# Optimization experiments

Hardware: AMD Instinct MI355X
Metric: run time of the kernel (lower is better)

Reference implementation:

```python
import jax, jax.numpy as jnp
import numpy as np

B, L, D = 4, 2048, 768
K, M, CK = 12, 1, 4            # heads, thetas, conv kernel size
H = D // (K * M)               # 64
DIM_MEM = K * H                # 768
DIM_EXPAND = H * 3             # 192
DSH = DIM_EXPAND * 2           # 384 swiglu head dim
DST = K * DSH                  # 4608
DIM_FUSED = DIM_MEM + K + DST  # 5388
THETA_MIN, THETA_MAX = 1e-3, 3.0


def setup_inputs() -> dict:
    key = jax.random.key(0)
    ks = jax.random.split(key, 5)
    x = jax.random.normal(ks[0], (B, L, D), jnp.float32)
    W_in = jax.random.normal(ks[1], (D, DIM_FUSED), jnp.float32) * 0.02
    conv_w = jax.random.normal(ks[2], (CK, DIM_MEM + K), jnp.float32) * 0.2  # depthwise taps
    rms_scale = jnp.ones((H,), jnp.float32)
    # theta_raw init (M==1 branch): inverse-sigmoid of geomspace grid
    grid = np.geomspace(THETA_MIN, THETA_MAX, K).reshape(1, 1, K, 1, 1)
    base = np.tile(grid, (1, 1, 1, H, 1))
    u = np.clip((base - THETA_MIN) / (THETA_MAX - THETA_MIN), 1e-4, 1 - 1e-4)
    theta_raw = jnp.asarray(np.log(u) - np.log(1.0 - u), jnp.float32)
    decay_slopes = jnp.asarray(np.log(np.exp(np.geomspace(1e-3, 0.1, K)) - 1.0), jnp.float32)
    score_scale = jnp.ones((K,), jnp.float32)
    tanh_scale = jnp.ones((K,), jnp.float32)
    W_sw = jax.random.normal(ks[3], (2 * K * H * M, DST), jnp.float32) * 0.02
    W_out = jax.random.normal(ks[4], (K * DIM_EXPAND, D), jnp.float32) * 0.02
    return {"x": x, "W_in": W_in, "conv_w": conv_w, "rms_scale": rms_scale,
            "theta_raw": theta_raw, "decay_slopes": decay_slopes,
            "score_scale": score_scale, "tanh_scale": tanh_scale,
            "W_sw": W_sw, "W_out": W_out}


def reference(x, W_in, conv_w, rms_scale, theta_raw, decay_slopes,
              score_scale, tanh_scale, W_sw, W_out):
    # fused in-projection
    z_fused = jnp.einsum('bld,df->blf', x, W_in)
    z_mem = z_fused[..., :DIM_MEM + K]
    skip_direct = z_fused[..., DIM_MEM + K:]
    # causal depthwise conv (kernel size CK, left pad CK-1)
    zp = jnp.pad(z_mem, ((0, 0), (CK - 1, 0), (0, 0)))
    z_conv = sum(zp[:, j:j + L, :] * conv_w[j] for j in range(CK))
    z_mem = jax.nn.silu(z_conv)
    # memory keys + RMSNorm over H
    k_val = z_mem[..., :DIM_MEM].reshape(B, L, K, H)
    k_val = k_val * jax.lax.rsqrt(jnp.mean(k_val * k_val, axis=-1, keepdims=True) + 1e-6) * rms_scale
    s_raw = z_mem[..., DIM_MEM:]  # (B, L, K)
    # theta (M == 1)
    theta = THETA_MIN + (THETA_MAX - THETA_MIN) * jax.nn.sigmoid(theta_raw)  # (1,1,K,H,1)
    # decay time weights (num_anchor_heads == 0, maxlen == L)
    pos = jnp.arange(L, dtype=jnp.float32)
    slopes = jax.nn.softplus(decay_slopes).reshape(1, 1, K)
    dist = jnp.maximum(jnp.float32(L - 1) - pos, 0.0)
    log_time_weight = -slopes * dist[None, :, None]  # (1, L, K)
    log_p = jnp.clip(score_scale[None, None, :] * s_raw, -10.0, 10.0)
    p_w = jnp.exp(log_p + log_time_weight)  # (B, L, K)
    # characteristic-function encoding
    k5 = k_val[..., None]  # (B, L, K, H, 1)
    phi = jnp.tanh(k5 * tanh_scale.reshape(1, 1, K, 1, 1)) * theta
    kvw = k5 * p_w[..., None, None]
    re = kvw * jnp.cos(phi)
    im = kvw * jnp.sin(phi)
    # fused causal cumulative accumulation
    flat = K * H * M
    stack = jnp.concatenate([p_w, re.reshape(B, L, flat), im.reshape(B, L, flat)], axis=-1)
    cs = jnp.cumsum(stack, axis=1)
    den_acc = cs[..., :K]
    re_acc = cs[..., K:K + flat].reshape(B, L, K, H, M)
    im_acc = cs[..., K + flat:].reshape(B, L, K, H, M)
    inv_den = (1.0 / jnp.maximum(den_acc, 1e-4))[..., None, None]
    summary_flat = jnp.stack([re_acc * inv_den, im_acc * inv_den], axis=-1).reshape(B, L, -1)
    # SwiGLU with skip
    y_spectral = jnp.einsum('bls,sf->blf', summary_flat, W_sw).reshape(B, L, K, DSH)
    y_skip = skip_direct.reshape(B, L, K, DSH)
    y_spec_val, y_spec_gate = jnp.split(y_spectral, 2, axis=-1)
    y_skip_val, y_skip_gate = jnp.split(y_skip, 2, axis=-1)
    y_act = (y_spec_val + y_skip_val) * jax.nn.silu(y_spec_gate + y_skip_gate)
    out = jnp.einsum('blf,fd->bld', y_act.reshape(B, L, -1), W_out)
    return out
```

## Files before the change

kernel.cpp:

```cpp
#include <hip/hip_runtime.h>
#include <hip/hip_bf16.h>

#define B_       4
#define L_       2048
#define D_       768
#define K_       12
#define H_       64
#define CK_      4
#define DIM_MEM_ 768
#define DMK      780
#define NT       (B_*L_)
#define NSUM     1536
#define NACT     2304
#define NCHUNK   16
#define CHLEN    (L_/NCHUNK)
#define PSTRIDE  132

typedef __attribute__((ext_vector_type(8))) short          bf16x8;
typedef __attribute__((ext_vector_type(8))) unsigned short u16x8;
typedef __attribute__((ext_vector_type(4))) float          f32x4;

__device__ __forceinline__ ushort f2bf(float v) {
    __hip_bfloat16 h = __float2bfloat16(v);
    return *reinterpret_cast<ushort*>(&h);
}
__device__ __forceinline__ float tanh_fast(float x) {
    float t = __expf(-2.f * fabsf(x));
    float r = (1.f - t) / (1.f + t);
    return copysignf(r, x);
}

struct PrepJobs {
    const float* W[6];
    ushort*      out[6];
    int ldw[6], Kd[6], colbase[6], remap[6], ntx[6];
    int start[7];
    const float* cast_in;
    ushort*      cast_out;
    int n4;
};

__global__ __launch_bounds__(256)
void prep_all(PrepJobs J)
{
    int blk = blockIdx.x;
    if (blk >= J.start[6]) {
        int i = (blk - J.start[6]) * 256 + threadIdx.x;
        if (i < J.n4) {
            float4 v = reinterpret_cast<const float4*>(J.cast_in)[i];
            ushort4 o;
            o.x = f2bf(v.x); o.y = f2bf(v.y); o.z = f2bf(v.z); o.w = f2bf(v.w);
            reinterpret_cast<ushort4*>(J.cast_out)[i] = o;
        }
        return;
    }
    int j = 0;
    while (blk >= J.start[j + 1]) ++j;
    int rel = blk - J.start[j];
    int ntx = J.ntx[j];
    int n0 = (rel % ntx) * 32, k0 = (rel / ntx) * 32;
    const float* W = J.W[j];
    int ldw = J.ldw[j], Kd = J.Kd[j], colbase = J.colbase[j], remap = J.remap[j];
    ushort* out = J.out[j];

    __shared__ float tile[32][33];
    int tx = threadIdx.x & 31, ty = threadIdx.x >> 5;
    int n = n0 + tx;
    int c = colbase + (remap ? (n/192)*384 + (n%192) : n);
    #pragma unroll
    for (int r = 0; r < 4; ++r)
        tile[ty + r*8][tx] = W[(size_t)(k0 + ty + r*8) * ldw + c];
    __syncthreads();
    #pragma unroll
    for (int r = 0; r < 4; ++r)
        out[(size_t)(n0 + ty + r*8) * Kd + k0 + tx] = f2bf(tile[tx][ty + r*8]);
}

__global__ __launch_bounds__(256)
void gemm_bf16_mfma(const ushort* __restrict__ A, const ushort* __restrict__ BT,
                    float* __restrict__ C, int Kd, int N, int ldc)
{
    __shared__ ushort As[128*64];
    __shared__ ushort Bs[128*64];
    int tid = threadIdx.x, lane = tid & 63;
    int lr = lane & 15, quad = lane >> 4;
    int wave = tid >> 6;
    int wr = (wave >> 1) * 64, wc = (wave & 1) * 64;
    int m0 = blockIdx.y * 128, n0 = blockIdx.x * 128;

    f32x4 acc[4][4] = {};

    int srow = tid >> 3;
    int tc   = tid & 7;
    const ushort* gA = A  + (size_t)(m0 + srow) * Kd + tc * 8;
    const ushort* gB = BT + (size_t)(n0 + srow) * Kd + tc * 8;
    int woff = srow * 64 + ((tc ^ (srow & 7)) * 8);
    int rx = lr & 7;

    for (int k0 = 0; k0 < Kd; k0 += 64) {
        u16x8 a[4], b[4];
        #pragma unroll
        for (int p = 0; p < 4; ++p) {
            a[p] = *reinterpret_cast<const u16x8*>(gA + (size_t)(32*p) * Kd);
            b[p] = *reinterpret_cast<const u16x8*>(gB + (size_t)(32*p) * Kd);
        }
        gA += 64; gB += 64;
        __syncthreads();
        #pragma unroll
        for (int p = 0; p < 4; ++p) {
            *reinterpret_cast<u16x8*>(As + woff + p*2048) = a[p];
            *reinterpret_cast<u16x8*>(Bs + woff + p*2048) = b[p];
        }
        __syncthreads();
        #pragma unroll
        for (int ks = 0; ks < 2; ++ks) {
            bf16x8 af[4], bf[4];
            #pragma unroll
            for (int i = 0; i < 4; ++i) {
                int ca = ((ks*4 + quad) ^ rx) * 8;
                af[i] = *reinterpret_cast<const bf16x8*>(As + (wr + i*16 + lr) * 64 + ca);
                bf[i] = *reinterpret_cast<const bf16x8*>(Bs + (wc + i*16 + lr) * 64 + ca);
            }
            #pragma unroll
            for (int i = 0; i < 4; ++i)
                #pragma unroll
                for (int j = 0; j < 4; ++j)
                    acc[i][j] = __builtin_amdgcn_mfma_f32_16x16x32_bf16(
                                    af[i], bf[j], acc[i][j], 0, 0, 0);
        }
    }

    #pragma unroll
    for (int i = 0; i < 4; ++i)
        #pragma unroll
        for (int j = 0; j < 4; ++j)
            #pragma unroll
            for (int r = 0; r < 4; ++r) {
                int row = m0 + wr + i*16 + quad*4 + r;
                int col = n0 + wc + j*16 + lr;
                if (col < N)
                    C[(size_t)row * ldc + col] = acc[i][j][r];
            }
}

__global__ __launch_bounds__(256)
void gemm2_mfma(const ushort* __restrict__ Sm, const ushort* __restrict__ Xb,
                const ushort* __restrict__ WsV, const ushort* __restrict__ WsG,
                const ushort* __restrict__ WiV, const ushort* __restrict__ WiG,
                ushort* __restrict__ yact)
{
    __shared__ ushort As[128*64];
    __shared__ ushort Bv[64*64];
    __shared__ ushort Bg[64*64];
    int tid = threadIdx.x, lane = tid & 63;
    int lr = lane & 15, quad = lane >> 4;
    int wave = tid >> 6;
    int wr = (wave >> 1) * 64, wc = (wave & 1) * 32;
    int m0 = blockIdx.y * 128, n0 = blockIdx.x * 64;

    f32x4 av[4][2] = {}, ag[4][2] = {};

    int srow = tid >> 3;
    int tc   = tid & 7;
    int woff = srow * 64 + ((tc ^ (srow & 7)) * 8);
    int rx = lr & 7;

    #pragma unroll 1
    for (int phase = 0; phase < 2; ++phase) {
        const ushort* Ap  = phase ? Xb  : Sm;
        const ushort* Bvp = phase ? WiV : WsV;
        const ushort* Bgp = phase ? WiG : WsG;
        int Kd = phase ? 768 : 1536;

        const ushort* gA = Ap  + (size_t)(m0 + srow) * Kd + tc * 8;
        const ushort* gv = Bvp + (size_t)(n0 + srow) * Kd + tc * 8;
        const ushort* gg = Bgp + (size_t)(n0 + srow) * Kd + tc * 8;

        for (int k0 = 0; k0 < Kd; k0 += 64) {
            u16x8 a[4], v2[2], g2[2];
            #pragma unroll
            for (int p = 0; p < 4; ++p)
                a[p] = *reinterpret_cast<const u16x8*>(gA + (size_t)(32*p) * Kd);
            #pragma unroll
            for (int p = 0; p < 2; ++p) {
                v2[p] = *reinterpret_cast<const u16x8*>(gv + (size_t)(32*p) * Kd);
                g2[p] = *reinterpret_cast<const u16x8*>(gg + (size_t)(32*p) * Kd);
            }
            gA += 64; gv += 64; gg += 64;
            __syncthreads();
            #pragma unroll
            for (int p = 0; p < 4; ++p)
                *reinterpret_cast<u16x8*>(As + woff + p*2048) = a[p];
            #pragma unroll
            for (int p = 0; p < 2; ++p) {
                *reinterpret_cast<u16x8*>(Bv + woff + p*2048) = v2[p];
                *reinterpret_cast<u16x8*>(Bg + woff + p*2048) = g2[p];
            }
            __syncthreads();
            #pragma unroll
            for (int ks = 0; ks < 2; ++ks) {
                bf16x8 af[4], bvf[2], bgf[2];
                #pragma unroll
                for (int i = 0; i < 4; ++i) {
                    int ca = ((ks*4 + quad) ^ rx) * 8;
                    af[i] = *reinterpret_cast<const bf16x8*>(As + (wr + i*16 + lr) * 64 + ca);
                }
                #pragma unroll
                for (int j = 0; j < 2; ++j) {
                    int ca = ((ks*4 + quad) ^ rx) * 8;
                    bvf[j] = *reinterpret_cast<const bf16x8*>(Bv + (wc + j*16 + lr) * 64 + ca);
                    bgf[j] = *reinterpret_cast<const bf16x8*>(Bg + (wc + j*16 + lr) * 64 + ca);
                }
                #pragma unroll
                for (int i = 0; i < 4; ++i)
                    #pragma unroll
                    for (int j = 0; j < 2; ++j) {
                        av[i][j] = __builtin_amdgcn_mfma_f32_16x16x32_bf16(
                                       af[i], bvf[j], av[i][j], 0, 0, 0);
                        ag[i][j] = __builtin_amdgcn_mfma_f32_16x16x32_bf16(
                                       af[i], bgf[j], ag[i][j], 0, 0, 0);
                    }
            }
        }
    }

    #pragma unroll
    for (int i = 0; i < 4; ++i)
        #pragma unroll
        for (int j = 0; j < 2; ++j)
            #pragma unroll
            for (int r = 0; r < 4; ++r) {
                int row = m0 + wr + i*16 + quad*4 + r;
                int col = n0 + wc + j*16 + lr;
                float v = av[i][j][r], g = ag[i][j][r];
                float y = v * (g / (1.f + __expf(-g)));
                yact[(size_t)row * NACT + col] = f2bf(y);
            }
}

__global__ __launch_bounds__(256)
void token_kernel(const float* __restrict__ zmem, const float* __restrict__ conv_w,
                  const float* __restrict__ rms_scale, const float* __restrict__ theta_raw,
                  const float* __restrict__ dslopes, const float* __restrict__ sscale,
                  const float* __restrict__ tscale,
                  float* __restrict__ pw, float* __restrict__ re, float* __restrict__ im)
{
    int t = blockIdx.x;
    int b = t >> 11;
    int l = t & (L_ - 1);
    int tid = threadIdx.x;
    int h = tid & 63, kg = tid >> 6;

    __shared__ float s_pw[K_];

    if (tid < K_) {
        float acc = 0.f;
        #pragma unroll
        for (int j = 0; j < CK_; ++j) {
            int ll = l - (CK_ - 1) + j;
            if (ll >= 0)
                acc += zmem[(size_t)(b*L_ + ll)*DMK + DIM_MEM_ + tid]
                     * conv_w[j*DMK + DIM_MEM_ + tid];
        }
        float s  = acc / (1.f + expf(-acc));
        float lp = sscale[tid] * s;
        lp = fminf(10.f, fmaxf(-10.f, lp));
        float slope = log1pf(expf(dslopes[tid]));
        s_pw[tid] = expf(lp - slope * (float)(L_ - 1 - l));
    }

    float kv[3];
    #pragma unroll
    for (int q = 0; q < 3; ++q) {
        int kk = kg + q*4;
        int c = kk*H_ + h;
        float acc = 0.f;
        #pragma unroll
        for (int j = 0; j < CK_; ++j) {
            int ll = l - (CK_ - 1) + j;
            if (ll >= 0)
                acc += zmem[(size_t)(b*L_ + ll)*DMK + c] * conv_w[j*DMK + c];
        }
        kv[q] = acc / (1.f + __expf(-acc));
    }
    __syncthreads();

    #pragma unroll
    for (int q = 0; q < 3; ++q) {
        int kk = kg + q*4;
        float v = kv[q];
        float ss = v * v;
        #pragma unroll
        for (int off = 32; off > 0; off >>= 1)
            ss += __shfl_xor(ss, off, 64);
        float kn = v * rsqrtf(ss * (1.f/64.f) + 1e-6f) * rms_scale[h];
        float th = 0.001f + 2.999f * (1.f / (1.f + __expf(-theta_raw[kk*H_ + h])));
        float phi = tanh_fast(kn * tscale[kk]) * th;
        float kvw = kn * s_pw[kk];
        re[(size_t)t*(K_*H_) + kk*H_ + h] = kvw * __cosf(phi);
        im[(size_t)t*(K_*H_) + kk*H_ + h] = kvw * __sinf(phi);
    }
    if (tid < K_) pw[(size_t)t*K_ + tid] = s_pw[tid];
}

__global__ __launch_bounds__(128)
void scan_sums(const float* __restrict__ pw, const float* __restrict__ re,
               const float* __restrict__ im, float* __restrict__ part)
{
    int blk = blockIdx.x;
    int chunk = blk & (NCHUNK - 1);
    int bk = blk >> 4;
    int k = bk % K_;
    int b = bk / K_;
    int tid = threadIdx.x;
    int h = tid & 63;
    const float* __restrict__ src = (tid >> 6) ? im : re;
    int l0 = chunk * CHLEN;

    size_t base  = ((size_t)(b*L_ + l0))*(K_*H_) + k*H_ + h;
    size_t dbase = ((size_t)(b*L_ + l0))*K_ + k;
    float s = 0.f, ds = 0.f;
    for (int i0 = 0; i0 < CHLEN; i0 += 8) {
        float v[8], d[8];
        #pragma unroll
        for (int j = 0; j < 8; ++j) {
            v[j] = src[base + (size_t)(i0 + j)*(K_*H_)];
            d[j] = pw [dbase + (size_t)(i0 + j)*K_];
        }
        #pragma unroll
        for (int j = 0; j < 8; ++j) { s += v[j]; ds += d[j]; }
    }
    size_t pb = ((size_t)bk * NCHUNK + chunk) * PSTRIDE;
    part[pb + tid] = s;
    if (tid == 0) part[pb + 128] = ds;
}

__global__ __launch_bounds__(128)
void scan_final(const float* __restrict__ pw, const float* __restrict__ re,
                const float* __restrict__ im, const float* __restrict__ part,
                ushort* __restrict__ summary)
{
    int blk = blockIdx.x;
    int chunk = blk & (NCHUNK - 1);
    int bk = blk >> 4;
    int k = bk % K_;
    int b = bk / K_;
    int tid = threadIdx.x;
    int h = tid & 63;
    int pi = tid >> 6;
    const float* __restrict__ src = pi ? im : re;
    int l0 = chunk * CHLEN;

    float acc = 0.f, dacc = 0.f;
    size_t pb0 = (size_t)bk * NCHUNK * PSTRIDE;
    for (int cn = 0; cn < chunk; ++cn) {
        acc  += part[pb0 + (size_t)cn*PSTRIDE + tid];
        dacc += part[pb0 + (size_t)cn*PSTRIDE + 128];
    }

    size_t base  = ((size_t)(b*L_ + l0))*(K_*H_) + k*H_ + h;
    size_t dbase = ((size_t)(b*L_ + l0))*K_ + k;
    int outch = 2*(k*H_ + h) + pi;
    for (int i0 = 0; i0 < CHLEN; i0 += 8) {
        float v[8], d[8];
        #pragma unroll
        for (int j = 0; j < 8; ++j) {
            v[j] = src[base + (size_t)(i0 + j)*(K_*H_)];
            d[j] = pw [dbase + (size_t)(i0 + j)*K_];
        }
        #pragma unroll
        for (int j = 0; j < 8; ++j) {
            acc += v[j]; dacc += d[j];
            float inv = 1.f / fmaxf(dacc, 1e-4f);
            summary[((size_t)(b*L_ + l0 + i0 + j))*NSUM + outch] = f2bf(acc * inv);
        }
    }
}

extern "C" void kernel_launch(void* const* d_in, const int* in_sizes, int n_in,
                              void* d_out, int out_size, void* d_ws, size_t ws_size,
                              hipStream_t stream)
{
    const float* x         = (const float*)d_in[0];
    const float* W_in      = (const float*)d_in[1];
    const float* conv_w    = (const float*)d_in[2];
    const float* rms_scale = (const float*)d_in[3];
    const float* theta_raw = (const float*)d_in[4];
    const float* dslopes   = (const float*)d_in[5];
    const float* sscale    = (const float*)d_in[6];
    const float* tscale    = (const float*)d_in[7];
    const float* W_sw      = (const float*)d_in[8];
    const float* W_out     = (const float*)d_in[9];
    float* out = (float*)d_out;
    char* ws   = (char*)d_ws;

    float*  zmem    = (float*) (ws + 0);
    ushort* summary = (ushort*)(ws + 0);
    float*  pw      = (float*) (ws + 25559040);
    float*  re      = (float*) (ws + 25952256);
    float*  im      = (float*) (ws + 51118080);
    ushort* yact    = (ushort*)(ws + 25952256);
    float*  part    = (float*) (ws + 76283904);
    ushort* xb      = (ushort*)(ws + 76689408);
    ushort* WiV     = (ushort*)(ws + 89272320);
    ushort* WiG     = (ushort*)(ws + 92811264);
    ushort* WsV     = (ushort*)(ws + 96350208);
    ushort* WsG     = (ushort*)(ws + 103428096);
    ushort* WoT     = (ushort*)(ws + 110505984);
    ushort* WimT    = (ushort*)(ws + 114044928);

    PrepJobs J;
    J.W[0]=W_in;  J.out[0]=WiV;  J.ldw[0]=5388; J.Kd[0]=768;  J.colbase[0]=780; J.remap[0]=1; J.ntx[0]=72;
    J.W[1]=W_in;  J.out[1]=WiG;  J.ldw[1]=5388; J.Kd[1]=768;  J.colbase[1]=972; J.remap[1]=1; J.ntx[1]=72;
    J.W[2]=W_sw;  J.out[2]=WsV;  J.ldw[2]=4608; J.Kd[2]=1536; J.colbase[2]=0;   J.remap[2]=1; J.ntx[2]=72;
    J.W[3]=W_sw;  J.out[3]=WsG;  J.ldw[3]=4608; J.Kd[3]=1536; J.colbase[3]=192; J.remap[3]=1; J.ntx[3]=72;
    J.W[4]=W_out; J.out[4]=WoT;  J.ldw[4]=768;  J.Kd[4]=2304; J.colbase[4]=0;   J.remap[4]=0; J.ntx[4]=24;
    J.W[5]=W_in;  J.out[5]=WimT; J.ldw[5]=5388; J.Kd[5]=768;  J.colbase[5]=0;   J.remap[5]=0; J.ntx[5]=28;
    int tiles[6] = {72*24, 72*24, 72*48, 72*48, 24*72, 28*24};
    J.start[0] = 0;
    for (int j = 0; j < 6; ++j) J.start[j+1] = J.start[j] + tiles[j];
    J.cast_in = x; J.cast_out = xb; J.n4 = NT*D_/4;
    int nblk = J.start[6] + (J.n4 + 255)/256;

    dim3 blk(256);
    prep_all<<<dim3(nblk), blk, 0, stream>>>(J);
    gemm_bf16_mfma<<<dim3(7, 64), blk, 0, stream>>>(xb, WimT, zmem, 768, 780, 780);
    token_kernel<<<dim3(NT), blk, 0, stream>>>(zmem, conv_w, rms_scale, theta_raw,
                                               dslopes, sscale, tscale, pw, re, im);
    scan_sums <<<dim3(B_*K_*NCHUNK), dim3(128), 0, stream>>>(pw, re, im, part);
    scan_final<<<dim3(B_*K_*NCHUNK), dim3(128), 0, stream>>>(pw, re, im, part, summary);
    gemm2_mfma<<<dim3(NACT/64, NT/128), blk, 0, stream>>>(summary, xb,
                                                          WsV, WsG, WiV, WiG, yact);
    gemm_bf16_mfma<<<dim3(6, 64), blk, 0, stream>>>(yact, WoT, out, 2304, 768, 768);
}
```

Before: 436.3 us.

## Rewrite SwiGLU GEMM with async LDS loads, larger tiles and interleaved weights

New measurement: 423.3 us. 1.03x faster.

```diff
diff --git a/kernel.cpp b/kernel.cpp
--- a/kernel.cpp
+++ b/kernel.cpp
@@ -66,7 +66,13 @@
     __shared__ float tile[32][33];
     int tx = threadIdx.x & 31, ty = threadIdx.x >> 5;
     int n = n0 + tx;
-    int c = colbase + (remap ? (n/192)*384 + (n%192) : n);
+    int c;
+    if (remap) {
+        int grp = n >> 5, which = (n >> 4) & 1, nn = (grp << 4) + (n & 15);
+        c = colbase + (nn / 192) * 384 + which * 192 + (nn % 192);
+    } else {
+        c = colbase + n;
+    }
     #pragma unroll
     for (int r = 0; r < 4; ++r)
         tile[ty + r*8][tx] = W[(size_t)(k0 + ty + r*8) * ldw + c];
@@ -143,97 +149,172 @@
             }
 }
 
-__global__ __launch_bounds__(256)
-void gemm2_mfma(const ushort* __restrict__ Sm, const ushort* __restrict__ Xb,
-                const ushort* __restrict__ WsV, const ushort* __restrict__ WsG,
-                const ushort* __restrict__ WiV, const ushort* __restrict__ WiG,
-                ushort* __restrict__ yact)
-{
-    __shared__ ushort As[128*64];
-    __shared__ ushort Bv[64*64];
-    __shared__ ushort Bg[64*64];
-    int tid = threadIdx.x, lane = tid & 63;
-    int lr = lane & 15, quad = lane >> 4;
-    int wave = tid >> 6;
-    int wr = (wave >> 1) * 64, wc = (wave & 1) * 32;
-    int m0 = blockIdx.y * 128, n0 = blockIdx.x * 64;
-
-    f32x4 av[4][2] = {}, ag[4][2] = {};
-
-    int srow = tid >> 3;
-    int tc   = tid & 7;
-    int woff = srow * 64 + ((tc ^ (srow & 7)) * 8);
-    int rx = lr & 7;
+#define G2NKT 36
+
+#define GLOAD16(gp, dp) __builtin_amdgcn_global_load_lds( \
+    (__attribute__((address_space(1))) const void*)(gp),  \
+    (__attribute__((address_space(3))) void*)(dp), 16, 0, 0)
+
+__device__ __forceinline__ void g2_stageA(ushort* lds_, int kt,
+                                          const ushort* pAs, const ushort* pAx,
+                                          int wave, int part)
+{
+    int ktc = kt > (G2NKT-1) ? (G2NKT-1) : kt;
+    const ushort* g; size_t kd;
+    if (ktc < 24) { g = pAs + ktc*64;      kd = 1536; }
+    else          { g = pAx + (ktc-24)*64; kd = 768;  }
+    g += (size_t)(part * 128) * kd;
+    ushort* d = lds_ + (kt & 1) * 16384 + part * 8192 + wave * 512;
+    GLOAD16(g,           d);
+    GLOAD16(g + 64*kd,   d + 4096);
+}
+
+__device__ __forceinline__ void g2_stageB(ushort* lds_, int kt,
+                                          const ushort* pBs, const ushort* pBx,
+                                          int wave)
+{
+    int ktc = kt > (G2NKT-1) ? (G2NKT-1) : kt;
+    const ushort* g; size_t kd;
+    if (ktc < 24) { g = pBs + ktc*64;      kd = 1536; }
+    else          { g = pBx + (ktc-24)*64; kd = 768;  }
+    ushort* d = lds_ + 32768 + (kt & 1) * 12288 + wave * 512;
+    GLOAD16(g,           d);
+    GLOAD16(g + 64*kd,   d + 4096);
+    GLOAD16(g + 128*kd,  d + 8192);
+}
+
+__global__ __launch_bounds__(512, 2)
+void gemm2_8ph(const ushort* __restrict__ Sm, const ushort* __restrict__ Xb,
+               const ushort* __restrict__ WsC, const ushort* __restrict__ WiC,
+               ushort* __restrict__ yact)
+{
+    __shared__ ushort lds[57344];
+    const int tid  = threadIdx.x;
+    const int lane = tid & 63, wave = tid >> 6;
+    const int lr = lane & 15, quad = lane >> 4, rx = lr & 7;
+    const int wr = (wave >> 1) * 64;
+    const int wc = (wave & 1) * 96;
+    const int m0 = blockIdx.y * 256, n0 = blockIdx.x * 192;
+
+    const int sr = tid >> 3;
+    const int sc = (tid & 7) ^ (sr & 7);
+    const ushort* pAs = Sm  + (size_t)(m0 + sr) * 1536 + sc * 8;
+    const ushort* pAx = Xb  + (size_t)(m0 + sr) * 768  + sc * 8;
+    const ushort* pBs = WsC + (size_t)(n0 + sr) * 1536 + sc * 8;
+    const ushort* pBx = WiC + (size_t)(n0 + sr) * 768  + sc * 8;
+
+    f32x4 acc[4][6] = {};
+    bf16x8 af[4][2];
+    const int ca0 = (quad ^ rx) * 8;
+    const int ca1 = ((4 + quad) ^ rx) * 8;
+
+    g2_stageA(lds, 0, pAs, pAx, wave, 0);
+    g2_stageA(lds, 0, pAs, pAx, wave, 1);
+    g2_stageB(lds, 0, pBs, pBx, wave);
+    g2_stageA(lds, 1, pAs, pAx, wave, 0);
+    g2_stageA(lds, 1, pAs, pAx, wave, 1);
+    asm volatile("s_waitcnt vmcnt(4)" ::: "memory");
+    __builtin_amdgcn_s_barrier();
 
     #pragma unroll 1
-    for (int phase = 0; phase < 2; ++phase) {
-        const ushort* Ap  = phase ? Xb  : Sm;
-        const ushort* Bvp = phase ? WiV : WsV;
-        const ushort* Bgp = phase ? WiG : WsG;
-        int Kd = phase ? 768 : 1536;
-
-        const ushort* gA = Ap  + (size_t)(m0 + srow) * Kd + tc * 8;
-        const ushort* gv = Bvp + (size_t)(n0 + srow) * Kd + tc * 8;
-        const ushort* gg = Bgp + (size_t)(n0 + srow) * Kd + tc * 8;
-
-        for (int k0 = 0; k0 < Kd; k0 += 64) {
-            u16x8 a[4], v2[2], g2[2];
-            #pragma unroll
-            for (int p = 0; p < 4; ++p)
-                a[p] = *reinterpret_cast<const u16x8*>(gA + (size_t)(32*p) * Kd);
-            #pragma unroll
-            for (int p = 0; p < 2; ++p) {
-                v2[p] = *reinterpret_cast<const u16x8*>(gv + (size_t)(32*p) * Kd);
-                g2[p] = *reinterpret_cast<const u16x8*>(gg + (size_t)(32*p) * Kd);
-            }
-            gA += 64; gv += 64; gg += 64;
-            __syncthreads();
-            #pragma unroll
-            for (int p = 0; p < 4; ++p)
-                *reinterpret_cast<u16x8*>(As + woff + p*2048) = a[p];
-            #pragma unroll
-            for (int p = 0; p < 2; ++p) {
-                *reinterpret_cast<u16x8*>(Bv + woff + p*2048) = v2[p];
-                *reinterpret_cast<u16x8*>(Bg + woff + p*2048) = g2[p];
-            }
-            __syncthreads();
-            #pragma unroll
-            for (int ks = 0; ks < 2; ++ks) {
-                bf16x8 af[4], bvf[2], bgf[2];
-                #pragma unroll
-                for (int i = 0; i < 4; ++i) {
-                    int ca = ((ks*4 + quad) ^ rx) * 8;
-                    af[i] = *reinterpret_cast<const bf16x8*>(As + (wr + i*16 + lr) * 64 + ca);
-                }
-                #pragma unroll
-                for (int j = 0; j < 2; ++j) {
-                    int ca = ((ks*4 + quad) ^ rx) * 8;
-                    bvf[j] = *reinterpret_cast<const bf16x8*>(Bv + (wc + j*16 + lr) * 64 + ca);
-                    bgf[j] = *reinterpret_cast<const bf16x8*>(Bg + (wc + j*16 + lr) * 64 + ca);
-                }
+    for (int g = 0; g < G2NKT; ++g) {
+        const ushort* Ab = lds + (g & 1) * 16384;
+        const ushort* Bb = lds + 32768 + (g & 1) * 12288;
+
+        {
+            #pragma unroll
+            for (int i = 0; i < 4; ++i) {
+                const ushort* p = Ab + (wr + i*16 + lr) * 64;
+                af[i][0] = *reinterpret_cast<const bf16x8*>(p + ca0);
+                af[i][1] = *reinterpret_cast<const bf16x8*>(p + ca1);
+            }
+            bf16x8 bfr[2][2];
+            #pragma unroll
+            for (int j = 0; j < 2; ++j) {
+                const ushort* p = Bb + (wc + j*16 + lr) * 64;
+                bfr[j][0] = *reinterpret_cast<const bf16x8*>(p + ca0);
+                bfr[j][1] = *reinterpret_cast<const bf16x8*>(p + ca1);
+            }
+            g2_stageB(lds, g + 1, pBs, pBx, wave);
+            __builtin_amdgcn_s_barrier();
+            asm volatile("s_waitcnt lgkmcnt(0)" ::: "memory");
+            __builtin_amdgcn_sched_barrier(0);
+            __builtin_amdgcn_s_setprio(1);
+            #pragma unroll
+            for (int ks = 0; ks < 2; ++ks)
                 #pragma unroll
                 for (int i = 0; i < 4; ++i)
                     #pragma unroll
-                    for (int j = 0; j < 2; ++j) {
-                        av[i][j] = __builtin_amdgcn_mfma_f32_16x16x32_bf16(
-                                       af[i], bvf[j], av[i][j], 0, 0, 0);
-                        ag[i][j] = __builtin_amdgcn_mfma_f32_16x16x32_bf16(
-                                       af[i], bgf[j], ag[i][j], 0, 0, 0);
-                    }
-            }
-        }
-    }
-
+                    for (int j = 0; j < 2; ++j)
+                        acc[i][j] = __builtin_amdgcn_mfma_f32_16x16x32_bf16(
+                                        af[i][ks], bfr[j][ks], acc[i][j], 0, 0, 0);
+            __builtin_amdgcn_s_setprio(0);
+            __builtin_amdgcn_s_barrier();
+        }
+        {
+            bf16x8 bfr[2][2];
+            #pragma unroll
+            for (int j = 0; j < 2; ++j) {
+                const ushort* p = Bb + (wc + (2 + j)*16 + lr) * 64;
+                bfr[j][0] = *reinterpret_cast<const bf16x8*>(p + ca0);
+                bfr[j][1] = *reinterpret_cast<const bf16x8*>(p + ca1);
+            }
+            g2_stageA(lds, g + 2, pAs, pAx, wave, 0);
+            __builtin_amdgcn_s_barrier();
+            asm volatile("s_waitcnt lgkmcnt(0)" ::: "memory");
+            __builtin_amdgcn_sched_barrier(0);
+            __builtin_amdgcn_s_setprio(1);
+            #pragma unroll
+            for (int ks = 0; ks < 2; ++ks)
+                #pragma unroll
+                for (int i = 0; i < 4; ++i)
+                    #pragma unroll
+                    for (int j = 0; j < 2; ++j)
+                        acc[i][2 + j] = __builtin_amdgcn_mfma_f32_16x16x32_bf16(
+                                        af[i][ks], bfr[j][ks], acc[i][2 + j], 0, 0, 0);
+            __builtin_amdgcn_s_setprio(0);
+            __builtin_amdgcn_s_barrier();
+        }
+        {
+            bf16x8 bfr[2][2];
+            #pragma unroll
+            for (int j = 0; j < 2; ++j) {
+                const ushort* p = Bb + (wc + (4 + j)*16 + lr) * 64;
+                bfr[j][0] = *reinterpret_cast<const bf16x8*>(p + ca0);
+                bfr[j][1] = *reinterpret_cast<const bf16x8*>(p + ca1);
+            }
+            g2_stageA(lds, g + 2, pAs, pAx, wave, 1);
+            asm volatile("s_waitcnt vmcnt(4)" ::: "memory");
+            __builtin_amdgcn_s_barrier();
+            asm volatile("s_waitcnt lgkmcnt(0)" ::: "memory");
+            __builtin_amdgcn_sched_barrier(0);
+            __builtin_amdgcn_s_setprio(1);
+            #pragma unroll
+            for (int ks = 0; ks < 2; ++ks)
+                #pragma unroll
+                for (int i = 0; i < 4; ++i)
+                    #pragma unroll
+                    for (int j = 0; j < 2; ++j)
+                        acc[i][4 + j] = __builtin_amdgcn_mfma_f32_16x16x32_bf16(
+                                        af[i][ks], bfr[j][ks], acc[i][4 + j], 0, 0, 0);
+            __builtin_amdgcn_s_setprio(0);
+            __builtin_amdgcn_s_barrier();
+        }
+    }
+    asm volatile("s_waitcnt vmcnt(0)" ::: "memory");
+
+    const int vg0 = (n0 + wc) >> 5;
     #pragma unroll
     for (int i = 0; i < 4; ++i)
         #pragma unroll
-        for (int j = 0; j < 2; ++j)
+        for (int p = 0; p < 3; ++p)
             #pragma unroll
             for (int r = 0; r < 4; ++r) {
                 int row = m0 + wr + i*16 + quad*4 + r;
-                int col = n0 + wc + j*16 + lr;
-                float v = av[i][j][r], g = ag[i][j][r];
-                float y = v * (g / (1.f + __expf(-g)));
+                int col = (vg0 + p)*16 + lr;
+                float v  = acc[i][2*p][r];
+                float gt = acc[i][2*p + 1][r];
+                float y = v * (gt / (1.f + __expf(-gt)));
                 yact[(size_t)row * NACT + col] = f2bf(y);
             }
 }
@@ -402,23 +483,21 @@
     ushort* yact    = (ushort*)(ws + 25952256);
     float*  part    = (float*) (ws + 76283904);
     ushort* xb      = (ushort*)(ws + 76689408);
-    ushort* WiV     = (ushort*)(ws + 89272320);
-    ushort* WiG     = (ushort*)(ws + 92811264);
-    ushort* WsV     = (ushort*)(ws + 96350208);
-    ushort* WsG     = (ushort*)(ws + 103428096);
+    ushort* WiCat   = (ushort*)(ws + 89272320);
+    ushort* WsCat   = (ushort*)(ws + 96350208);
     ushort* WoT     = (ushort*)(ws + 110505984);
     ushort* WimT    = (ushort*)(ws + 114044928);
 
-    PrepJobs J;
-    J.W[0]=W_in;  J.out[0]=WiV;  J.ldw[0]=5388; J.Kd[0]=768;  J.colbase[0]=780; J.remap[0]=1; J.ntx[0]=72;
-    J.W[1]=W_in;  J.out[1]=WiG;  J.ldw[1]=5388; J.Kd[1]=768;  J.colbase[1]=972; J.remap[1]=1; J.ntx[1]=72;
-    J.W[2]=W_sw;  J.out[2]=WsV;  J.ldw[2]=4608; J.Kd[2]=1536; J.colbase[2]=0;   J.remap[2]=1; J.ntx[2]=72;
-    J.W[3]=W_sw;  J.out[3]=WsG;  J.ldw[3]=4608; J.Kd[3]=1536; J.colbase[3]=192; J.remap[3]=1; J.ntx[3]=72;
-    J.W[4]=W_out; J.out[4]=WoT;  J.ldw[4]=768;  J.Kd[4]=2304; J.colbase[4]=0;   J.remap[4]=0; J.ntx[4]=24;
-    J.W[5]=W_in;  J.out[5]=WimT; J.ldw[5]=5388; J.Kd[5]=768;  J.colbase[5]=0;   J.remap[5]=0; J.ntx[5]=28;
-    int tiles[6] = {72*24, 72*24, 72*48, 72*48, 24*72, 28*24};
+    PrepJobs J{};
+    J.W[0]=W_in;  J.out[0]=WiCat; J.ldw[0]=5388; J.Kd[0]=768;  J.colbase[0]=780; J.remap[0]=1; J.ntx[0]=144;
+    J.W[1]=W_sw;  J.out[1]=WsCat; J.ldw[1]=4608; J.Kd[1]=1536; J.colbase[1]=0;   J.remap[1]=1; J.ntx[1]=144;
+    J.W[2]=W_out; J.out[2]=WoT;   J.ldw[2]=768;  J.Kd[2]=2304; J.colbase[2]=0;   J.remap[2]=0; J.ntx[2]=24;
+    J.W[3]=W_in;  J.out[3]=WimT;  J.ldw[3]=5388; J.Kd[3]=768;  J.colbase[3]=0;   J.remap[3]=0; J.ntx[3]=28;
+    int tiles[4] = {144*24, 144*48, 24*72, 28*24};
     J.start[0] = 0;
-    for (int j = 0; j < 6; ++j) J.start[j+1] = J.start[j] + tiles[j];
+    for (int j = 0; j < 4; ++j) J.start[j+1] = J.start[j] + tiles[j];
+    J.start[5] = J.start[4];
+    J.start[6] = J.start[4];
     J.cast_in = x; J.cast_out = xb; J.n4 = NT*D_/4;
     int nblk = J.start[6] + (J.n4 + 255)/256;
 
@@ -429,7 +508,6 @@
                                                dslopes, sscale, tscale, pw, re, im);
     scan_sums <<<dim3(B_*K_*NCHUNK), dim3(128), 0, stream>>>(pw, re, im, part);
     scan_final<<<dim3(B_*K_*NCHUNK), dim3(128), 0, stream>>>(pw, re, im, part, summary);
-    gemm2_mfma<<<dim3(NACT/64, NT/128), blk, 0, stream>>>(summary, xb,
-                                                          WsV, WsG, WiV, WiG, yact);
+    gemm2_8ph<<<dim3(24, 32), dim3(512), 0, stream>>>(summary, xb, WsCat, WiCat, yact);
     gemm_bf16_mfma<<<dim3(6, 64), blk, 0, stream>>>(yact, WoT, out, 2304, 768, 768);
 }
```
